# Kernel tuning notes

Hardware: AMD Instinct MI355X
Metric: run time of the kernel (lower is better)

The kernel has to match this reference:

```python
import jax, jax.numpy as jnp
import numpy as np

B, S, C = 8, 2048, 1024
DROPOUT_RATE = 0.1


def setup_inputs() -> dict:
    key = jax.random.key(0)
    k1, k2, k3 = jax.random.split(key, 3)
    x = jax.random.normal(k1, (B, S, C), dtype=jnp.float32)
    # Fixed orthogonal projection buffer, as in __init__: U from SVD of a random matrix
    rand_mat = jax.random.normal(k2, (C, C), dtype=jnp.float32)
    U, _, _ = jnp.linalg.svd(rand_mat)
    U = U.astype(jnp.float32)
    # Base random permutation of [0, C)
    perm = jax.random.permutation(k3, C).astype(jnp.int32)
    # Stand-in for random.randint(0, 1000), fixed for determinism
    randint = 123
    return {"x": x, "U": U, "perm": perm, "randint": randint}


def reference(x, U, perm, randint):
    # channel_dim == -1, so the transpose in the original forward is a no-op.
    rand_scale = (DROPOUT_RATE / (1.0 - DROPOUT_RATE)) ** 0.5
    n = x.shape[-1]
    b = x.size // n
    # _randperm_like: per-row permutation ans[b_, i] = perm[i] * (6*randint*b_ + 1) mod n.
    # Reduce the multiplier mod n first so int32 arithmetic never overflows
    # (math is identical since (a*b) % n == (a*(b%n)) % n).
    batch_rand = (jnp.arange(b, dtype=jnp.int32) * (randint * 6) + 1) % n  # [b]
    ans = (perm[None, :] * batch_rand[:, None]) % n                        # [b, n]
    ans = ans.reshape(x.shape)                                             # same shape as x

    x_g = jnp.take_along_axis(x, ans, axis=-1)   # gather per-row permuted channels
    y = jnp.matmul(x_g, U)                        # shared (C,C) projection
    # scatter_(-1, ans, y) places y[..., j] at position ans[..., j]; since ans is a
    # permutation per row, this equals gathering y with the inverse permutation.
    inv = jnp.argsort(ans, axis=-1)
    x_next = jnp.take_along_axis(y, inv, axis=-1)
    return x_next * rand_scale + x
```

## Files before the change

### kernel.cpp

```cpp
#include <hip/hip_runtime.h>
#include <hip/hip_bf16.h>

#define WS_UT    ((size_t)0)
#define WS_XG    ((size_t)2*1024*1024)

typedef __attribute__((ext_vector_type(8))) short short8;
typedef __attribute__((ext_vector_type(4))) float floatx4;

__device__ __forceinline__ void load_lds16(const void* g, void* l) {
  __builtin_amdgcn_global_load_lds(
      (const __attribute__((address_space(1))) void*)g,
      (__attribute__((address_space(3))) void*)l, 16, 0, 0);
}

__device__ __forceinline__ unsigned short f2bf(float f) {
  __hip_bfloat16 h = __float2bfloat16(f);
  return __builtin_bit_cast(unsigned short, h);
}
__device__ __forceinline__ float bf2f(unsigned short u) {
  return __uint_as_float(((unsigned)u) << 16);
}

__global__ void __launch_bounds__(256) prep_gather_k(const float* __restrict__ U,
                                                     const float* __restrict__ x,
                                                     const int* __restrict__ perm,
                                                     const int* __restrict__ prand,
                                                     unsigned short* __restrict__ ut,
                                                     unsigned short* __restrict__ xg) {
  __shared__ __align__(16) char smem[64 * 65 * 4];
  if (blockIdx.x < 256) {
    float (*tile)[65] = (float (*)[65])smem;
    const int tn = (blockIdx.x & 15) * 64;
    const int tk = (blockIdx.x >> 4) * 64;
    const int r = threadIdx.x >> 6;
    const int c = threadIdx.x & 63;
    for (int s = 0; s < 16; ++s)
      tile[s * 4 + r][c] = U[(size_t)(tk + s * 4 + r) * 1024 + tn + c];
    __syncthreads();
    for (int s = 0; s < 16; ++s)
      ut[(size_t)(tn + s * 4 + r) * 1024 + tk + c] = f2bf(tile[c][s * 4 + r]);
    return;
  }
  float (*xrow)[1024] = (float (*)[1024])smem;
  const int w = threadIdx.x >> 6, lane = threadIdx.x & 63;
  const int row = (blockIdx.x - 256) * 4 + w;
  const unsigned mult = ((unsigned)prand[0] * 6u) & 1023u;
  const unsigned br = (((unsigned)row & 1023u) * mult + 1u) & 1023u;
  const float* xr = x + (size_t)row * 1024;
  unsigned short* xo = xg + (size_t)row * 1024;
  for (int t = 0; t < 4; ++t) {
    floatx4 v = *(const floatx4*)(xr + t * 256 + lane * 4);
    *(floatx4*)(&xrow[w][t * 256 + lane * 4]) = v;
  }
  __syncthreads();
  for (int t = 0; t < 4; ++t) {
    int i0 = t * 256 + lane * 4;
    int4 p = *(const int4*)(perm + i0);
    ushort4 o;
    o.x = f2bf(xrow[w][((unsigned)p.x * br) & 1023u]);
    o.y = f2bf(xrow[w][((unsigned)p.y * br) & 1023u]);
    o.z = f2bf(xrow[w][((unsigned)p.z * br) & 1023u]);
    o.w = f2bf(xrow[w][((unsigned)p.w * br) & 1023u]);
    *(ushort4*)(xo + i0) = o;
  }
}

__global__ void __launch_bounds__(512, 1) gemm_scatter_k(
    const unsigned short* __restrict__ xg,
    const unsigned short* __restrict__ ut,
    const int* __restrict__ perm,
    const int* __restrict__ prand,
    float* __restrict__ out) {
  __shared__ __align__(16) char smem[65536];
  const int tid = threadIdx.x;
  const int w = tid >> 6, lane = tid & 63;
  const int m = lane & 15, q = lane >> 4;
  const int R0 = blockIdx.x * 64;
  const int wn = w * 128;

  const int x3 = m & 7;
  const int qq = q ^ (x3 & 3);
  const int sf = x3 >> 2;
  const int offA0 = m * 128 + (qq + sf * 4) * 16;
  const int offA1 = m * 128 + (qq + 4 - sf * 4) * 16;

  const int sr = lane >> 3, sslot = lane & 7;
  const unsigned short* asrc =
      xg + (size_t)(R0 + w * 8 + sr) * 1024 + (size_t)((sslot ^ sr) * 8);
  char* adst0 = smem + w * 1024 + lane * 16;

  const unsigned short* bb[8];
#pragma unroll
  for (int jj = 0; jj < 8; ++jj)
    bb[jj] = ut + (size_t)(wn + jj * 16 + m) * 1024 + q * 8;

  floatx4 acc[4][8];
#pragma unroll
  for (int i = 0; i < 4; ++i)
#pragma unroll
    for (int jj = 0; jj < 8; ++jj) acc[i][jj] = (floatx4)0.0f;

  load_lds16(asrc, adst0);
  load_lds16(asrc + 64, adst0 + 8192);
  short8 bcur[8];
#pragma unroll
  for (int jj = 0; jj < 8; ++jj) bcur[jj] = *(const short8*)(bb[jj]);
  __syncthreads();

#pragma unroll
  for (int kt = 0; kt < 16; ++kt) {
    const char* Ac = smem + (kt & 3) * 8192;
    short8 bodd[8];
#pragma unroll
    for (int jj = 0; jj < 8; ++jj)
      bodd[jj] = *(const short8*)(bb[jj] + kt * 64 + 32);
    short8 a0[4];
#pragma unroll
    for (int i = 0; i < 4; ++i) a0[i] = *(const short8*)(Ac + i * 2048 + offA0);
#pragma unroll
    for (int i = 0; i < 4; ++i)
#pragma unroll
      for (int jj = 0; jj < 8; ++jj)
        acc[i][jj] = __builtin_amdgcn_mfma_f32_16x16x32_bf16(bcur[jj], a0[i],
                                                             acc[i][jj], 0, 0, 0);
    if (kt < 15) {
#pragma unroll
      for (int jj = 0; jj < 8; ++jj)
        bcur[jj] = *(const short8*)(bb[jj] + (kt + 1) * 64);
    }
    if (kt < 14)
      load_lds16(asrc + (size_t)(kt + 2) * 64, adst0 + ((kt + 2) & 3) * 8192);
    short8 a1[4];
#pragma unroll
    for (int i = 0; i < 4; ++i) a1[i] = *(const short8*)(Ac + i * 2048 + offA1);
#pragma unroll
    for (int i = 0; i < 4; ++i)
#pragma unroll
      for (int jj = 0; jj < 8; ++jj)
        acc[i][jj] = __builtin_amdgcn_mfma_f32_16x16x32_bf16(bodd[jj], a1[i],
                                                             acc[i][jj], 0, 0, 0);
    if (kt < 15) {
      __builtin_amdgcn_sched_barrier(0);
      __builtin_amdgcn_s_barrier();
      __builtin_amdgcn_sched_barrier(0);
    }
  }
  __syncthreads();

  const unsigned mult = ((unsigned)prand[0] * 6u) & 1023u;
  const float rs = 0.33333334f;
  float* sbuf = (float*)smem;
#pragma unroll
  for (int i = 0; i < 4; ++i) {
    const int row = R0 + i * 16 + m;
    const unsigned br = (((unsigned)row & 1023u) * mult + 1u) & 1023u;
    const unsigned short* xr = xg + (size_t)row * 1024;
#pragma unroll
    for (int jj = 0; jj < 8; ++jj) {
      const int j0 = wn + jj * 16 + q * 4;
      const int4 p4 = *(const int4*)(perm + j0);
      const ushort4 x4 = *(const ushort4*)(xr + j0);
      sbuf[m * 1024 + (((unsigned)p4.x * br) & 1023u)] = rs * acc[i][jj][0] + bf2f(x4.x);
      sbuf[m * 1024 + (((unsigned)p4.y * br) & 1023u)] = rs * acc[i][jj][1] + bf2f(x4.y);
      sbuf[m * 1024 + (((unsigned)p4.z * br) & 1023u)] = rs * acc[i][jj][2] + bf2f(x4.z);
      sbuf[m * 1024 + (((unsigned)p4.w * br) & 1023u)] = rs * acc[i][jj][3] + bf2f(x4.w);
    }
    __syncthreads();
    float* orow0 = out + (size_t)(R0 + i * 16) * 1024;
#pragma unroll
    for (int v = 0; v < 8; ++v) {
      const int f = v * 512 + tid;
      *(floatx4*)(orow0 + ((f >> 8) * 1024 + (f & 255) * 4)) =
          *(const floatx4*)(sbuf + (size_t)f * 4);
    }
    if (i < 3) __syncthreads();
  }
}

extern "C" void kernel_launch(void* const* d_in, const int* in_sizes, int n_in,
                              void* d_out, int out_size, void* d_ws, size_t ws_size,
                              hipStream_t stream) {
  const float* x = (const float*)d_in[0];
  const float* U = (const float*)d_in[1];
  const int* perm = (const int*)d_in[2];
  const int* prand = (const int*)d_in[3];
  float* out = (float*)d_out;
  char* ws = (char*)d_ws;
  unsigned short* ut = (unsigned short*)(ws + WS_UT);
  unsigned short* xg = (unsigned short*)(ws + WS_XG);

  prep_gather_k<<<256 + 4096, 256, 0, stream>>>(U, x, perm, prand, ut, xg);
  gemm_scatter_k<<<256, 512, 0, stream>>>(xg, ut, perm, prand, out);
}
```

Before: 202.3 us.

## Stage B tiles through LDS with async loads and restructure GEMM pipeline

B (the transposed U) fragments now go through LDS with swizzled async global_load_lds copies instead of per-lane register loads. A uses a triple buffer, and explicit vmcnt waits plus setprio bracket the MFMA section. The scatter epilogue works on 8-row halves to fit inside the reorganised LDS, and dynamic shared memory is raised to about 152KB. The goal is better-coalesced B traffic and more load/compute overlap, at the cost of heavy LDS use, more barriers and hand-tuned wait counts that could be fragile.

Measured after the change: 165.7 us. -18.1%, faster.

```diff
diff --git a/kernel.cpp b/kernel.cpp
--- a/kernel.cpp
+++ b/kernel.cpp
@@ -65,34 +65,30 @@
   }
 }
 
-__global__ void __launch_bounds__(512, 1) gemm_scatter_k(
+__global__ void __launch_bounds__(512, 2) gemm_scatter_k(
     const unsigned short* __restrict__ xg,
     const unsigned short* __restrict__ ut,
     const int* __restrict__ perm,
     const int* __restrict__ prand,
     float* __restrict__ out) {
-  __shared__ __align__(16) char smem[65536];
+  extern __shared__ __align__(16) char smem[];
   const int tid = threadIdx.x;
   const int w = tid >> 6, lane = tid & 63;
   const int m = lane & 15, q = lane >> 4;
   const int R0 = blockIdx.x * 64;
   const int wn = w * 128;
 
-  const int x3 = m & 7;
-  const int qq = q ^ (x3 & 3);
-  const int sf = x3 >> 2;
-  const int offA0 = m * 128 + (qq + sf * 4) * 16;
-  const int offA1 = m * 128 + (qq + 4 - sf * 4) * 16;
-
-  const int sr = lane >> 3, sslot = lane & 7;
+  const int swz0 = (q ^ (m & 7)) * 16;
+  const int vA0 = m * 128 + swz0;
+  const int vA1 = vA0 ^ 64;
+  const int vB0 = 24576 + w * 16384 + m * 128 + swz0;
+  const int vB1 = vB0 ^ 64;
+
   const unsigned short* asrc =
-      xg + (size_t)(R0 + w * 8 + sr) * 1024 + (size_t)((sslot ^ sr) * 8);
-  char* adst0 = smem + w * 1024 + lane * 16;
-
-  const unsigned short* bb[8];
-#pragma unroll
-  for (int jj = 0; jj < 8; ++jj)
-    bb[jj] = ut + (size_t)(wn + jj * 16 + m) * 1024 + q * 8;
+      xg + (size_t)(R0 + (tid >> 3)) * 1024 + (size_t)(((tid & 7) ^ ((tid >> 3) & 7)) * 8);
+  const unsigned short* bsrc0 =
+      ut + (size_t)(wn + (lane >> 3)) * 1024 + (size_t)(((lane & 7) ^ (lane >> 3)) * 8);
+  char* bdst0 = smem + 24576 + w * 16384 + lane * 16;
 
   floatx4 acc[4][8];
 #pragma unroll
@@ -100,46 +96,58 @@
 #pragma unroll
     for (int jj = 0; jj < 8; ++jj) acc[i][jj] = (floatx4)0.0f;
 
-  load_lds16(asrc, adst0);
-  load_lds16(asrc + 64, adst0 + 8192);
-  short8 bcur[8];
-#pragma unroll
-  for (int jj = 0; jj < 8; ++jj) bcur[jj] = *(const short8*)(bb[jj]);
-  __syncthreads();
+  load_lds16(asrc, smem + tid * 16);
+#pragma unroll
+  for (int t = 0; t < 16; ++t)
+    load_lds16(bsrc0 + (size_t)t * 8192, bdst0 + t * 1024);
+  load_lds16(asrc + 64, smem + 8192 + tid * 16);
+  asm volatile("s_waitcnt vmcnt(1)" ::: "memory");
+  __builtin_amdgcn_sched_barrier(0);
+  __builtin_amdgcn_s_barrier();
+  __builtin_amdgcn_sched_barrier(0);
 
 #pragma unroll
   for (int kt = 0; kt < 16; ++kt) {
-    const char* Ac = smem + (kt & 3) * 8192;
-    short8 bodd[8];
-#pragma unroll
-    for (int jj = 0; jj < 8; ++jj)
-      bodd[jj] = *(const short8*)(bb[jj] + kt * 64 + 32);
+    const int ab = (kt % 3) * 8192;
     short8 a0[4];
 #pragma unroll
-    for (int i = 0; i < 4; ++i) a0[i] = *(const short8*)(Ac + i * 2048 + offA0);
-#pragma unroll
     for (int i = 0; i < 4; ++i)
-#pragma unroll
-      for (int jj = 0; jj < 8; ++jj)
-        acc[i][jj] = __builtin_amdgcn_mfma_f32_16x16x32_bf16(bcur[jj], a0[i],
-                                                             acc[i][jj], 0, 0, 0);
+      a0[i] = *(const short8*)(smem + ab + i * 2048 + vA0);
+    if (kt > 0) {
+      asm volatile("s_waitcnt vmcnt(1)" ::: "memory");
+      __builtin_amdgcn_sched_barrier(0);
+    }
+    __builtin_amdgcn_s_setprio(1);
+#pragma unroll
+    for (int jj = 0; jj < 8; ++jj) {
+      short8 b = *(const short8*)(smem + jj * 2048 + vB0);
+#pragma unroll
+      for (int i = 0; i < 4; ++i)
+        acc[i][jj] = __builtin_amdgcn_mfma_f32_16x16x32_bf16(b, a0[i], acc[i][jj], 0, 0, 0);
+    }
+    short8 a1[4];
+#pragma unroll
+    for (int i = 0; i < 4; ++i)
+      a1[i] = *(const short8*)(smem + ab + i * 2048 + vA1);
+#pragma unroll
+    for (int jj = 0; jj < 8; ++jj) {
+      short8 b = *(const short8*)(smem + jj * 2048 + vB1);
+#pragma unroll
+      for (int i = 0; i < 4; ++i)
+        acc[i][jj] = __builtin_amdgcn_mfma_f32_16x16x32_bf16(b, a1[i], acc[i][jj], 0, 0, 0);
+    }
+    __builtin_amdgcn_s_setprio(0);
     if (kt < 15) {
-#pragma unroll
-      for (int jj = 0; jj < 8; ++jj)
-        bcur[jj] = *(const short8*)(bb[jj] + (kt + 1) * 64);
-    }
-    if (kt < 14)
-      load_lds16(asrc + (size_t)(kt + 2) * 64, adst0 + ((kt + 2) & 3) * 8192);
-    short8 a1[4];
-#pragma unroll
-    for (int i = 0; i < 4; ++i) a1[i] = *(const short8*)(Ac + i * 2048 + offA1);
-#pragma unroll
-    for (int i = 0; i < 4; ++i)
-#pragma unroll
-      for (int jj = 0; jj < 8; ++jj)
-        acc[i][jj] = __builtin_amdgcn_mfma_f32_16x16x32_bf16(bodd[jj], a1[i],
-                                                             acc[i][jj], 0, 0, 0);
-    if (kt < 15) {
+      asm volatile("s_waitcnt lgkmcnt(0)" ::: "memory");
+      __builtin_amdgcn_sched_barrier(0);
+      const int k1 = (kt + 1) * 64;
+#pragma unroll
+      for (int t = 0; t < 16; ++t)
+        load_lds16(bsrc0 + (size_t)t * 8192 + k1, bdst0 + t * 1024);
+      if (kt < 14)
+        load_lds16(asrc + (size_t)(kt + 2) * 64, smem + ((kt + 2) % 3) * 8192 + tid * 16);
+      if (kt < 14) asm volatile("s_waitcnt vmcnt(17)" ::: "memory");
+      else         asm volatile("s_waitcnt vmcnt(16)" ::: "memory");
       __builtin_amdgcn_sched_barrier(0);
       __builtin_amdgcn_s_barrier();
       __builtin_amdgcn_sched_barrier(0);
@@ -149,31 +157,33 @@
 
   const unsigned mult = ((unsigned)prand[0] * 6u) & 1023u;
   const float rs = 0.33333334f;
-  float* sbuf = (float*)smem;
-#pragma unroll
-  for (int i = 0; i < 4; ++i) {
-    const int row = R0 + i * 16 + m;
-    const unsigned br = (((unsigned)row & 1023u) * mult + 1u) & 1023u;
-    const unsigned short* xr = xg + (size_t)row * 1024;
-#pragma unroll
-    for (int jj = 0; jj < 8; ++jj) {
-      const int j0 = wn + jj * 16 + q * 4;
-      const int4 p4 = *(const int4*)(perm + j0);
-      const ushort4 x4 = *(const ushort4*)(xr + j0);
-      sbuf[m * 1024 + (((unsigned)p4.x * br) & 1023u)] = rs * acc[i][jj][0] + bf2f(x4.x);
-      sbuf[m * 1024 + (((unsigned)p4.y * br) & 1023u)] = rs * acc[i][jj][1] + bf2f(x4.y);
-      sbuf[m * 1024 + (((unsigned)p4.z * br) & 1023u)] = rs * acc[i][jj][2] + bf2f(x4.z);
-      sbuf[m * 1024 + (((unsigned)p4.w * br) & 1023u)] = rs * acc[i][jj][3] + bf2f(x4.w);
+  float* sbuf = (float*)(smem + 24576);
+#pragma unroll
+  for (int p = 0; p < 8; ++p) {
+    const int i = p >> 1;
+    if ((m >> 3) == (p & 1)) {
+      const int r = i * 16 + m;
+      const unsigned br = (((unsigned)(R0 + r) & 1023u) * mult + 1u) & 1023u;
+      const unsigned short* xr = xg + (size_t)(R0 + r) * 1024;
+#pragma unroll
+      for (int jj = 0; jj < 8; ++jj) {
+        const int j0 = wn + jj * 16 + q * 4;
+        const int4 p4 = *(const int4*)(perm + j0);
+        const ushort4 x4 = *(const ushort4*)(xr + j0);
+        sbuf[((r & 7) << 10) + (((unsigned)p4.x * br) & 1023u)] = rs * acc[i][jj][0] + bf2f(x4.x);
+        sbuf[((r & 7) << 10) + (((unsigned)p4.y * br) & 1023u)] = rs * acc[i][jj][1] + bf2f(x4.y);
+        sbuf[((r & 7) << 10) + (((unsigned)p4.z * br) & 1023u)] = rs * acc[i][jj][2] + bf2f(x4.z);
+        sbuf[((r & 7) << 10) + (((unsigned)p4.w * br) & 1023u)] = rs * acc[i][jj][3] + bf2f(x4.w);
+      }
     }
     __syncthreads();
-    float* orow0 = out + (size_t)(R0 + i * 16) * 1024;
-#pragma unroll
-    for (int v = 0; v < 8; ++v) {
+    float* orow = out + (size_t)(R0 + p * 8) * 1024;
+#pragma unroll
+    for (int v = 0; v < 4; ++v) {
       const int f = v * 512 + tid;
-      *(floatx4*)(orow0 + ((f >> 8) * 1024 + (f & 255) * 4)) =
-          *(const floatx4*)(sbuf + (size_t)f * 4);
-    }
-    if (i < 3) __syncthreads();
+      *(floatx4*)(orow + (size_t)f * 4) = *(const floatx4*)(sbuf + (size_t)f * 4);
+    }
+    if (p < 7) __syncthreads();
   }
 }
 
@@ -189,6 +199,9 @@
   unsigned short* ut = (unsigned short*)(ws + WS_UT);
   unsigned short* xg = (unsigned short*)(ws + WS_XG);
 
+  hipFuncSetAttribute((const void*)gemm_scatter_k,
+                      hipFuncAttributeMaxDynamicSharedMemorySize, 155648);
+
   prep_gather_k<<<256 + 4096, 256, 0, stream>>>(U, x, perm, prand, ut, xg);
-  gemm_scatter_k<<<256, 512, 0, stream>>>(xg, ut, perm, prand, out);
-}
+  gemm_scatter_k<<<256, 512, 155648, stream>>>(xg, ut, perm, prand, out);
+}
```
